# Optimization experiments

Hardware: AMD Instinct MI355X
Metric: run time of the kernel (lower is better)

Reference implementation:

```python
import jax, jax.numpy as jnp
import numpy as np

N_NODES = 100000
N_EDGES = 1280000
D_IN = 64
D_HID = 64
D_OUT = 64


def sage_conv(x, src, dst, W_l, b_l, W_r):
    # PyG SAGEConv (aggr='mean', root_weight=True):
    #   out_i = W_l @ mean_{j in N(i)} x_j + b_l + W_r @ x_i
    msg = x[src]  # [E, d] gather of source-node features
    agg = jax.ops.segment_sum(msg, dst, num_segments=N_NODES)
    cnt = jax.ops.segment_sum(jnp.ones((src.shape[0],), x.dtype), dst,
                              num_segments=N_NODES)
    mean = agg / jnp.maximum(cnt, 1.0)[:, None]
    return mean @ W_l.T + b_l + x @ W_r.T


def setup_inputs() -> dict:
    key = jax.random.key(0)
    ks = jax.random.split(key, 8)
    x = jax.random.normal(ks[0], (N_NODES, D_IN), dtype=jnp.float32)
    edge_index = jax.random.randint(ks[1], (2, N_EDGES), 0, N_NODES,
                                    dtype=jnp.int64)
    s1 = 1.0 / np.sqrt(D_IN)
    s2 = 1.0 / np.sqrt(D_HID)
    W1_l = jax.random.uniform(ks[2], (D_HID, D_IN), jnp.float32, -s1, s1)
    b1 = jnp.zeros((D_HID,), jnp.float32)
    W1_r = jax.random.uniform(ks[3], (D_HID, D_IN), jnp.float32, -s1, s1)
    W2_l = jax.random.uniform(ks[4], (D_OUT, D_HID), jnp.float32, -s2, s2)
    b2 = jnp.zeros((D_OUT,), jnp.float32)
    W2_r = jax.random.uniform(ks[5], (D_OUT, D_HID), jnp.float32, -s2, s2)
    return {"x": x, "edge_index": edge_index,
            "W1_l": W1_l, "b1": b1, "W1_r": W1_r,
            "W2_l": W2_l, "b2": b2, "W2_r": W2_r}


def reference(x, edge_index, W1_l, b1, W1_r, W2_l, b2, W2_r):
    src, dst = edge_index[0], edge_index[1]
    h = sage_conv(x, src, dst, W1_l, b1, W1_r)
    h = jax.nn.relu(h)
    # dropout p=0.0 -> identity
    out = sage_conv(h, src, dst, W2_l, b2, W2_r)
    return out
```

## Files before the change

### kernel.cpp

```cpp
#include <hip/hip_runtime.h>

#define NN 100000
#define NE 1280000
#define D  64

#define BINSZ   512
#define NBIN    196
#define ESTRIDE 7168
#define CHUNK   4096
#define NT      (NN / 16)
#define NSHARD  16
#define NBUCKET (BINSZ * NSHARD)

#define SCATB   ((NE + CHUNK - 1) / CHUNK)
#define XBLKS   3125
#define WBLKS   64

typedef unsigned int   uint;
typedef unsigned short ushort;
typedef unsigned char  uchar;
typedef __attribute__((ext_vector_type(8))) short short8v;
typedef __attribute__((ext_vector_type(4))) float f32x4;

__device__ __forceinline__ ushort f2bf(float f) {
    uint u = __float_as_uint(f);
    uint r = (u + 0x7fffu + ((u >> 16) & 1u)) >> 16;
    return (ushort)r;
}
__device__ __forceinline__ float bf2f(ushort h) {
    return __uint_as_float(((uint)h) << 16);
}
__device__ __forceinline__ float bfhi_f(uint w) { return __uint_as_float(w & 0xffff0000u); }
__device__ __forceinline__ float bflo_f(uint w) { return __uint_as_float(w << 16); }
__device__ __forceinline__ uint packbf(float a, float b) {
    return (uint)f2bf(a) | ((uint)f2bf(b) << 16);
}

__global__ __launch_bounds__(256) void scatter_prep(
        const int* __restrict__ srcv, const int* __restrict__ dstv,
        int* __restrict__ bincur, uint* __restrict__ ecol,
        const float* __restrict__ x, uint* __restrict__ xb,
        const float* __restrict__ w0, const float* __restrict__ w1,
        const float* __restrict__ w2, const float* __restrict__ w3,
        ushort* __restrict__ hi, ushort* __restrict__ lo) {
    __shared__ uint  ebuf[CHUNK];
    __shared__ uchar bbuf[CHUNK];
    __shared__ int hist[256];
    __shared__ int hbase[256];
    __shared__ int gbase[256];

    const int bid = blockIdx.x;
    const int tid = threadIdx.x;

    if (bid >= SCATB) {
        if (bid < SCATB + XBLKS) {
            const int g = (bid - SCATB) * 256 + tid;
            const float4* xp = (const float4*)x + (size_t)g * 2;
            const float4 v0 = xp[0], v1 = xp[1];
            uint4 o;
            o.x = packbf(v0.x, v0.y);
            o.y = packbf(v0.z, v0.w);
            o.z = packbf(v1.x, v1.y);
            o.w = packbf(v1.z, v1.w);
            ((uint4*)xb)[g] = o;
        } else {
            const int g = (bid - SCATB - XBLKS) * 256 + tid;
            if (g < 4 * 4096) {
                const int m = g >> 12;
                const float* src = (m == 0) ? w0 : (m == 1) ? w1 : (m == 2) ? w2 : w3;
                const float f = src[g & 4095];
                const ushort h = f2bf(f);
                hi[g] = h;
                lo[g] = f2bf(f - bf2f(h));
            }
        }
        return;
    }

    const int base = bid * CHUNK;

    hist[tid] = 0;
    __syncthreads();

    uint pk[16];
    int  bn[16], rk[16];
    #pragma unroll
    for (int r = 0; r < 16; ++r) {
        const int e = base + r * 256 + tid;
        if (e < NE) {
            const int d = dstv[e];
            bn[r] = d >> 9;
            pk[r] = ((uint)srcv[e] << 9) | (uint)(d & 511);
            rk[r] = atomicAdd(&hist[bn[r]], 1);
        } else {
            bn[r] = -1;
        }
    }
    __syncthreads();

    const int v = hist[tid];
    hbase[tid] = v;
    __syncthreads();
    for (int d = 1; d < 256; d <<= 1) {
        const int t = (tid >= d) ? hbase[tid - d] : 0;
        __syncthreads();
        hbase[tid] += t;
        __syncthreads();
    }
    hbase[tid] -= v;
    if (tid < NBIN && v > 0)
        gbase[tid] = atomicAdd(&bincur[tid], v);
    __syncthreads();

    #pragma unroll
    for (int r = 0; r < 16; ++r) {
        if (bn[r] >= 0) {
            const int p = hbase[bn[r]] + rk[r];
            ebuf[p] = pk[r];
            bbuf[p] = (uchar)bn[r];
        }
    }
    __syncthreads();

    const int n = min(CHUNK, NE - base);
    for (int i = tid; i < n; i += 256) {
        const int b   = bbuf[i];
        const int pib = gbase[b] + (i - hbase[b]);
        if (pib < ESTRIDE)
            ecol[(size_t)b * ESTRIDE + pib] = ebuf[i];
    }
}

__global__ __launch_bounds__(1024) void binsort(const uint* __restrict__ ecol,
                                                const int* __restrict__ bincur,
                                                int* __restrict__ col,
                                                int* __restrict__ offs) {
    __shared__ int hist[NBUCKET];
    __shared__ int wpart[16];
    __shared__ int gdst_s;

    const int b = blockIdx.x;
    const int t = threadIdx.x;
    const int lane = t & 63;
    const int wv   = t >> 6;
    const int n    = min(bincur[b], ESTRIDE);
    const int gsrc = b * ESTRIDE;

    #pragma unroll
    for (int j = 0; j < NBUCKET / 1024; ++j) hist[t + j * 1024] = 0;

    if (wv == 0) {
        int s = 0;
        for (int i = lane; i < b; i += 64) s += min(bincur[i], ESTRIDE);
        #pragma unroll
        for (int d = 1; d < 64; d <<= 1) s += __shfl_xor(s, d);
        if (lane == 0) gdst_s = s;
    }
    __syncthreads();
    const int gdst = gdst_s;

    const int NIT = ESTRIDE / 1024;
    int bk[NIT], sv[NIT], rk[NIT];
    #pragma unroll
    for (int it = 0; it < NIT; ++it) {
        const int i = t + it * 1024;
        if (i < n) {
            const uint e = ecol[gsrc + i];
            bk[it] = (int)(((e & 511u) << 4) | (e >> 22));
            sv[it] = (int)(e >> 9);
            rk[it] = atomicAdd(&hist[bk[it]], 1);
        } else {
            bk[it] = -1;
        }
    }
    __syncthreads();

    int own[8], s = 0;
    #pragma unroll
    for (int j = 0; j < 8; ++j) { own[j] = hist[t * 8 + j]; s += own[j]; }
    int incl = s;
    #pragma unroll
    for (int d = 1; d < 64; d <<= 1) {
        const int up = __shfl_up(incl, d);
        if (lane >= d) incl += up;
    }
    if (lane == 63) wpart[wv] = incl;
    __syncthreads();
    if (wv == 0) {
        int p = (lane < 16) ? wpart[lane] : 0;
        int ip = p;
        #pragma unroll
        for (int d = 1; d < 16; d <<= 1) {
            const int up = __shfl_up(ip, d);
            if (lane >= d) ip += up;
        }
        if (lane < 16) wpart[lane] = ip - p;
    }
    __syncthreads();
    int run = wpart[wv] + incl - s;
    #pragma unroll
    for (int j = 0; j < 8; ++j) { const int c = own[j]; hist[t * 8 + j] = run; run += c; }
    __syncthreads();

    if (t < BINSZ) {
        const int node = b * BINSZ + t;
        if (node < NN) offs[node] = gdst + hist[t * 16];
        if (b == NBIN - 1 && node == NN - 1) offs[NN] = gdst + n;
    }

    #pragma unroll
    for (int it = 0; it < NIT; ++it)
        if (bk[it] >= 0)
            col[gdst + hist[bk[it]] + rk[it]] = sv[it];
}

__device__ __forceinline__ void gload(int (&id)[4], uint4 (&r0)[4], uint4 (&r1)[4],
                                      int k0, int deg, const int* __restrict__ col,
                                      int o0, const uint* __restrict__ gsrc, int q) {
    #pragma unroll
    for (int u = 0; u < 4; ++u) {
        const int k = k0 + u;
        id[u] = (k < deg) ? col[o0 + k] : -1;
    }
    #pragma unroll
    for (int u = 0; u < 4; ++u) {
        if (id[u] >= 0) {
            const uint* row = gsrc + (size_t)id[u] * 32;
            r0[u] = *(const uint4*)(row + 4 * q);
            r1[u] = *(const uint4*)(row + 16 + 4 * q);
        }
    }
}

__device__ __forceinline__ void gconsume(const int (&id)[4], const uint4 (&r0)[4],
                                         const uint4 (&r1)[4], float (&acc)[16]) {
    #pragma unroll
    for (int u = 0; u < 4; ++u) {
        if (id[u] >= 0) {
            uint w;
            w = r0[u].x; acc[0]  += bflo_f(w); acc[1]  += bfhi_f(w);
            w = r0[u].y; acc[2]  += bflo_f(w); acc[3]  += bfhi_f(w);
            w = r0[u].z; acc[4]  += bflo_f(w); acc[5]  += bfhi_f(w);
            w = r0[u].w; acc[6]  += bflo_f(w); acc[7]  += bfhi_f(w);
            w = r1[u].x; acc[8]  += bflo_f(w); acc[9]  += bfhi_f(w);
            w = r1[u].y; acc[10] += bflo_f(w); acc[11] += bfhi_f(w);
            w = r1[u].z; acc[12] += bflo_f(w); acc[13] += bfhi_f(w);
            w = r1[u].w; acc[14] += bflo_f(w); acc[15] += bfhi_f(w);
        }
    }
}

template<int SELF_BF16, int WF32, int WB16>
__global__ __launch_bounds__(256) void fused_layer(
        const uint*   __restrict__ gsrc,
        const float*  __restrict__ selff,
        const ushort* __restrict__ selfb,
        const int*    __restrict__ col,
        const int*    __restrict__ offs,
        const ushort* __restrict__ wl_hi, const ushort* __restrict__ wl_lo,
        const ushort* __restrict__ wr_hi, const ushort* __restrict__ wr_lo,
        const float*  __restrict__ bias,
        float* __restrict__ outf, ushort* __restrict__ outb,
        int do_relu)
{
    const int l   = threadIdx.x & 63;
    const int wid = (blockIdx.x * 256 + threadIdx.x) >> 6;
    if (wid >= NT) return;
    const int m16   = l & 15;
    const int q     = l >> 4;
    const int koff  = q * 8;
    const int mbase = wid * 16;
    const int node  = mbase + m16;

    const int o0  = offs[node];
    const int deg = offs[node + 1] - o0;

    float acc[16];
    #pragma unroll
    for (int j = 0; j < 16; ++j) acc[j] = 0.f;

    int idA[4], idB[4];
    uint4 a0[4], a1[4], b0[4], b1[4];

    if (__any(deg > 0)) {
        gload(idA, a0, a1, 0, deg, col, o0, gsrc, q);
        int k = 4;
        for (;;) {
            const bool more = __any(k < deg);
            if (more) gload(idB, b0, b1, k, deg, col, o0, gsrc, q);
            gconsume(idA, a0, a1, acc);
            if (!more) break;
            k += 4;
            const bool more2 = __any(k < deg);
            if (more2) gload(idA, a0, a1, k, deg, col, o0, gsrc, q);
            gconsume(idB, b0, b1, acc);
            if (!more2) break;
            k += 4;
        }
    }

    const float inv = 1.0f / (float)max(deg, 1);
    short8v am[2];
    #pragma unroll
    for (int j = 0; j < 8; ++j) {
        am[0][j] = (short)f2bf(acc[j] * inv);
        am[1][j] = (short)f2bf(acc[8 + j] * inv);
    }

    short8v ashi[2], aslo[2];
    if (SELF_BF16) {
        ashi[0] = *(const short8v*)(selfb + (size_t)node * 64 + koff);
        ashi[1] = *(const short8v*)(selfb + (size_t)node * 64 + 32 + koff);
    } else {
        #pragma unroll
        for (int kk = 0; kk < 2; ++kk) {
            const float4* xp = (const float4*)(selff + (size_t)node * 64 + kk * 32 + koff);
            const float4 v0 = xp[0], v1 = xp[1];
            const float vv[8] = {v0.x, v0.y, v0.z, v0.w, v1.x, v1.y, v1.z, v1.w};
            #pragma unroll
            for (int j = 0; j < 8; ++j) {
                const ushort hb_ = f2bf(vv[j]);
                ashi[kk][j] = (short)hb_;
                aslo[kk][j] = (short)f2bf(vv[j] - bf2f(hb_));
            }
        }
    }

    #pragma unroll
    for (int nt = 0; nt < 4; ++nt) {
        f32x4 acc4 = {0.f, 0.f, 0.f, 0.f};
        #pragma unroll
        for (int kk = 0; kk < 2; ++kk) {
            const size_t wo = (size_t)(nt * 16 + m16) * 64 + kk * 32 + koff;
            const short8v bwlh = *(const short8v*)(wl_hi + wo);
            const short8v bwll = *(const short8v*)(wl_lo + wo);
            const short8v bwrh = *(const short8v*)(wr_hi + wo);
            const short8v bwrl = *(const short8v*)(wr_lo + wo);
            acc4 = __builtin_amdgcn_mfma_f32_16x16x32_bf16(am[kk],   bwlh, acc4, 0, 0, 0);
            acc4 = __builtin_amdgcn_mfma_f32_16x16x32_bf16(am[kk],   bwll, acc4, 0, 0, 0);
            acc4 = __builtin_amdgcn_mfma_f32_16x16x32_bf16(ashi[kk], bwrh, acc4, 0, 0, 0);
            if (!SELF_BF16)
                acc4 = __builtin_amdgcn_mfma_f32_16x16x32_bf16(aslo[kk], bwrh, acc4, 0, 0, 0);
            acc4 = __builtin_amdgcn_mfma_f32_16x16x32_bf16(ashi[kk], bwrl, acc4, 0, 0, 0);
        }
        const float bv = bias[nt * 16 + m16];
        #pragma unroll
        for (int r = 0; r < 4; ++r) {
            float v = acc4[r] + bv;
            if (do_relu) v = fmaxf(v, 0.f);
            const size_t oi = (size_t)(mbase + q * 4 + r) * 64 + nt * 16 + m16;
            if (WF32) outf[oi] = v;
            if (WB16) outb[oi] = f2bf(v);
        }
    }
}

extern "C" void kernel_launch(void* const* d_in, const int* in_sizes, int n_in,
                              void* d_out, int out_size, void* d_ws, size_t ws_size,
                              hipStream_t stream) {
    const float* x   = (const float*)d_in[0];
    const int*   ei  = (const int*)d_in[1];
    const float* W1l = (const float*)d_in[2];
    const float* b1  = (const float*)d_in[3];
    const float* W1r = (const float*)d_in[4];
    const float* W2l = (const float*)d_in[5];
    const float* b2  = (const float*)d_in[6];
    const float* W2r = (const float*)d_in[7];
    float*       out = (float*)d_out;

    const int* src = ei;
    const int* dst = ei + NE;

    char* p = (char*)d_ws;
    int*    bincur = (int*)p;    p += 1024;
    int*    col    = (int*)p;    p += (size_t)NE * 4;
    int*    offs   = (int*)p;    p += (size_t)(NN + 1) * 4 + 60;
    ushort* whi    = (ushort*)p; p += (size_t)4 * 4096 * 2;
    ushort* wlo    = (ushort*)p; p += (size_t)4 * 4096 * 2;
    uint*   xb     = (uint*)p;   p += (size_t)NN * 32 * 4;
    uint*   hb     = (uint*)p;   p += (size_t)NN * 32 * 4;
    uint*   ecol   = hb;

    const ushort* w1l_hi = whi;             const ushort* w1l_lo = wlo;
    const ushort* w1r_hi = whi + 4096;      const ushort* w1r_lo = wlo + 4096;
    const ushort* w2l_hi = whi + 2 * 4096;  const ushort* w2l_lo = wlo + 2 * 4096;
    const ushort* w2r_hi = whi + 3 * 4096;  const ushort* w2r_lo = wlo + 3 * 4096;

    hipMemsetAsync(bincur, 0, 1024, stream);

    scatter_prep<<<SCATB + XBLKS + WBLKS, 256, 0, stream>>>(
        src, dst, bincur, ecol, x, xb, W1l, W1r, W2l, W2r, whi, wlo);

    binsort<<<NBIN, 1024, 0, stream>>>(ecol, bincur, col, offs);

    fused_layer<0, 0, 1><<<(NT * 64 + 255) / 256, 256, 0, stream>>>(
        xb, x, nullptr, col, offs,
        w1l_hi, w1l_lo, w1r_hi, w1r_lo, b1, nullptr, (ushort*)hb, 1);

    fused_layer<1, 1, 0><<<(NT * 64 + 255) / 256, 256, 0, stream>>>(
        hb, nullptr, (const ushort*)hb, col, offs,
        w2l_hi, w2l_lo, w2r_hi, w2r_lo, b2, out, nullptr, 0);
}
```

Baseline: 244.4 us.

## Split neighbor gather of each node tile across two waves with LDS reduction

Each 16-node tile is now handled by a pair of wavefronts that take alternating 4-edge chunks of the neighbor lists. The two partial sums are combined through shared memory, and only the second wave goes on to the GEMM epilogue. The aim is to double the memory-level parallelism of the latency-bound gather. In exchange it adds an LDS round trip, a block barrier, and idle waves during the epilogue, and the block size rises to 512.

```diff
diff --git a/kernel.cpp b/kernel.cpp
--- a/kernel.cpp
+++ b/kernel.cpp
@@ -187,7 +187,7 @@
     if (lane == 63) wpart[wv] = incl;
     __syncthreads();
     if (wv == 0) {
-        int p = (lane < 16) ? wpart[lane] : 0;
+        const int p = (lane < 16) ? wpart[lane] : 0;
         int ip = p;
         #pragma unroll
         for (int d = 1; d < 16; d <<= 1) {
@@ -251,7 +251,7 @@
 }
 
 template<int SELF_BF16, int WF32, int WB16>
-__global__ __launch_bounds__(256) void fused_layer(
+__global__ __launch_bounds__(512) void fused_layer(
         const uint*   __restrict__ gsrc,
         const float*  __restrict__ selff,
         const ushort* __restrict__ selfb,
@@ -263,13 +263,19 @@
         float* __restrict__ outf, ushort* __restrict__ outb,
         int do_relu)
 {
-    const int l   = threadIdx.x & 63;
-    const int wid = (blockIdx.x * 256 + threadIdx.x) >> 6;
-    if (wid >= NT) return;
-    const int m16   = l & 15;
-    const int q     = l >> 4;
+    __shared__ float red[4][64 * 17];
+
+    const int t      = threadIdx.x;
+    const int lane   = t & 63;
+    const int wv     = t >> 6;
+    const int pairid = wv >> 1;
+    const int half   = wv & 1;
+    const int tile   = min(blockIdx.x * 4 + pairid, NT - 1);
+
+    const int m16   = lane & 15;
+    const int q     = lane >> 4;
     const int koff  = q * 8;
-    const int mbase = wid * 16;
+    const int mbase = tile * 16;
     const int node  = mbase + m16;
 
     const int o0  = offs[node];
@@ -281,23 +287,30 @@
 
     int idA[4], idB[4];
     uint4 a0[4], a1[4], b0[4], b1[4];
-
-    if (__any(deg > 0)) {
-        gload(idA, a0, a1, 0, deg, col, o0, gsrc, q);
-        int k = 4;
+    int k = half * 4;
+    if (__any(k < deg)) {
+        gload(idA, a0, a1, k, deg, col, o0, gsrc, q);
         for (;;) {
-            const bool more = __any(k < deg);
-            if (more) gload(idB, b0, b1, k, deg, col, o0, gsrc, q);
+            const bool more = __any(k + 8 < deg);
+            if (more) gload(idB, b0, b1, k + 8, deg, col, o0, gsrc, q);
             gconsume(idA, a0, a1, acc);
             if (!more) break;
-            k += 4;
-            const bool more2 = __any(k < deg);
-            if (more2) gload(idA, a0, a1, k, deg, col, o0, gsrc, q);
+            const bool more2 = __any(k + 16 < deg);
+            if (more2) gload(idA, a0, a1, k + 16, deg, col, o0, gsrc, q);
             gconsume(idB, b0, b1, acc);
             if (!more2) break;
-            k += 4;
-        }
-    }
+            k += 16;
+        }
+    }
+
+    if (half == 0) {
+        #pragma unroll
+        for (int j = 0; j < 16; ++j) red[pairid][lane * 17 + j] = acc[j];
+    }
+    __syncthreads();
+    if (half == 0) return;
+    #pragma unroll
+    for (int j = 0; j < 16; ++j) acc[j] += red[pairid][lane * 17 + j];
 
     const float inv = 1.0f / (float)max(deg, 1);
     short8v am[2];
@@ -393,11 +406,11 @@
 
     binsort<<<NBIN, 1024, 0, stream>>>(ecol, bincur, col, offs);
 
-    fused_layer<0, 0, 1><<<(NT * 64 + 255) / 256, 256, 0, stream>>>(
+    fused_layer<0, 0, 1><<<(NT + 3) / 4, 512, 0, stream>>>(
         xb, x, nullptr, col, offs,
         w1l_hi, w1l_lo, w1r_hi, w1r_lo, b1, nullptr, (ushort*)hb, 1);
 
-    fused_layer<1, 1, 0><<<(NT * 64 + 255) / 256, 256, 0, stream>>>(
+    fused_layer<1, 1, 0><<<(NT + 3) / 4, 512, 0, stream>>>(
         hb, nullptr, (const ushort*)hb, col, offs,
         w2l_hi, w2l_lo, w2r_hi, w2r_lo, b2, out, nullptr, 0);
 }
```

Result: slower. 251.8 us (+3.1%).
